# Kernel tuning notes

Measured on AMD Instinct MI355X. Metric: run time of the kernel, lower is better.

## Reference

```python
import jax, jax.numpy as jnp
import numpy as np
from jax import lax

BINS = 256
HSIG = 0.01
MS_WEIGHTS = np.array([0.0448, 0.2856, 0.3001, 0.2363, 0.1333], dtype=np.float32)


def _conv(x, w, b=None, pad='SAME', groups=1):
    out = lax.conv_general_dilated(x, w, (1, 1), pad,
                                   feature_group_count=groups,
                                   dimension_numbers=('NCHW', 'OIHW', 'NCHW'))
    if b is not None:
        out = out + b[None, :, None, None]
    return out


def _avg_pool(x, k):
    B, C, H, W = x.shape
    return x.reshape(B, C, H // k, k, W // k, k).mean(axis=(3, 5))


def _max_pool2(x):
    return lax.reduce_window(x, -jnp.inf, lax.max, (1, 1, 2, 2), (1, 1, 2, 2), 'VALID')


def _gauss_win():
    c = jnp.arange(11, dtype=jnp.float32) - 5.0
    g = jnp.exp(-(c * c) / (2.0 * 1.5 * 1.5))
    return g / g.sum()


def _gauss_filter(x, win):
    C = x.shape[1]
    wh = jnp.tile(win.reshape(1, 1, 11, 1), (C, 1, 1, 1))
    ww = jnp.tile(win.reshape(1, 1, 1, 11), (C, 1, 1, 1))
    x = _conv(x, wh, pad='VALID', groups=C)
    return _conv(x, ww, pad='VALID', groups=C)


def _ssim(X, Y, win):
    C1, C2 = 0.01 ** 2, 0.03 ** 2
    mu1 = _gauss_filter(X, win)
    mu2 = _gauss_filter(Y, win)
    s11 = _gauss_filter(X * X, win) - mu1 * mu1
    s22 = _gauss_filter(Y * Y, win) - mu2 * mu2
    s12 = _gauss_filter(X * Y, win) - mu1 * mu2
    cs = (2.0 * s12 + C2) / (s11 + s22 + C2)
    ssim = ((2.0 * mu1 * mu2 + C1) / (mu1 * mu1 + mu2 * mu2 + C1)) * cs
    return ssim.mean(axis=(2, 3)), cs.mean(axis=(2, 3))  # (B,C) each


def _ms_ssim(X, Y):
    win = _gauss_win()
    vals = []
    for i in range(5):
        s, c = _ssim(X, Y, win)
        vals.append(jax.nn.relu(s if i == 4 else c))
        if i < 4:
            X = _avg_pool(X, 2)
            Y = _avg_pool(Y, 2)
    v = jnp.stack(vals)  # (5,B,C)
    w = jnp.asarray(MS_WEIGHTS)[:, None, None]
    return jnp.prod(v ** w, axis=0).mean()


def _soft_hist(y, edges):
    # faithful to source: broadcast every pixel against 256 Gaussian bins,
    # sum over dim 0 (batch), then normalize to a distribution.
    h = jnp.exp(-0.5 * ((y[..., None] - edges) / HSIG) ** 2).sum(axis=0)  # (C,H,W,BINS)
    return h / h.sum()


def _vgg_feats(x, ws, bs):
    # VGG19 features[:16]: conv1_1..conv3_3, maxpool after conv idx 1 and 3.
    for i, (w, b) in enumerate(zip(ws, bs)):
        x = jax.nn.relu(_conv(x, w, b))
        if i in (1, 3):
            x = _max_pool2(x)
    return x


def combined_loss(y_true, y_pred, ws, bs):
    B, C, H, W = y_pred.shape
    diff = y_pred - y_true
    ad = jnp.abs(diff)
    # smooth L1 (beta=1)
    l1 = jnp.mean(jnp.where(ad < 1.0, 0.5 * diff * diff, ad - 0.5))
    # MS-SSIM loss
    msssim_l = 1.0 - _ms_ssim(y_true, y_pred)
    # VGG perceptual
    f1 = _vgg_feats(y_true, ws, bs)
    f2 = _vgg_feats(y_pred, ws, bs)
    perc = jnp.mean((f1 - f2) ** 2)
    # soft histogram
    edges = jnp.linspace(0.0, 1.0, BINS, dtype=jnp.float32)
    hist_l = jnp.mean(jnp.abs(_soft_hist(y_true, edges) - _soft_hist(y_pred, edges)))
    # PSNR loss: 40 - (-10*log10(mse))
    mse = jnp.mean(diff * diff)
    psnr_l = 40.0 + 10.0 * jnp.log10(mse)
    # color loss
    color_l = jnp.mean(jnp.abs(y_true.mean(axis=(1, 2, 3)) - y_pred.mean(axis=(1, 2, 3))))
    # exposure loss (16x16 avg pool of channel mean, target 0.6)
    exp_l = jnp.mean((_avg_pool(y_pred.mean(axis=1, keepdims=True), 16) - 0.6) ** 2)
    # illumination smoothness (counts faithful to source)
    hv = jnp.sum((y_pred[:, :, 1:, :] - y_pred[:, :, :-1, :]) ** 2)
    wv = jnp.sum((y_pred[:, :, :, 1:] - y_pred[:, :, :, :-1]) ** 2)
    ill = 2.0 * (hv / ((W - 1) * C) + wv / (W * (C - 1))) / B
    # spatial consistency: 4 neighbor-difference kernels on 4x4-pooled luminance
    K = jnp.array([[[0, 0, 0], [-1, 1, 0], [0, 0, 0]],
                   [[0, 0, 0], [0, 1, -1], [0, 0, 0]],
                   [[0, -1, 0], [0, 1, 0], [0, 0, 0]],
                   [[0, 0, 0], [0, 1, 0], [0, -1, 0]]], dtype=jnp.float32)[:, None]  # (4,1,3,3)
    op = _avg_pool(y_true.mean(axis=1, keepdims=True), 4)
    ep = _avg_pool(y_pred.mean(axis=1, keepdims=True), 4)
    spat = jnp.sum((_conv(op, K) - _conv(ep, K)) ** 2, axis=1, keepdims=True)  # (B,1,H/4,W/4)
    total = (1.0 * l1 + 0.06 * perc + 0.05 * hist_l + 0.0083 * psnr_l
             + 0.25 * color_l + 0.5 * msssim_l + 0.1 * exp_l + 0.1 * ill + 0.1 * spat)
    return jnp.mean(total)


def setup_inputs() -> dict:
    key = jax.random.key(0)
    ks = jax.random.split(key, 16)
    B, H, W = 2, 224, 224
    y_true = jax.random.uniform(ks[0], (B, 3, H, W), dtype=jnp.float32)
    y_pred = jax.random.uniform(ks[1], (B, 3, H, W), dtype=jnp.float32)
    chans = [(64, 3), (64, 64), (128, 64), (128, 128), (256, 128), (256, 256), (256, 256)]
    inp = {'y_true': y_true, 'y_pred': y_pred}
    for i, (co, ci) in enumerate(chans):
        std = float(np.sqrt(2.0 / (ci * 9)))
        inp[f'w{i}'] = jax.random.normal(ks[2 + i], (co, ci, 3, 3), dtype=jnp.float32) * std
        inp[f'b{i}'] = jnp.zeros((co,), dtype=jnp.float32)
    return inp


def reference(y_true, y_pred, w0, w1, w2, w3, w4, w5, w6, b0, b1, b2, b3, b4, b5, b6):
    ws = [w0, w1, w2, w3, w4, w5, w6]
    bs = [b0, b1, b2, b3, b4, b5, b6]
    return combined_loss(y_true, y_pred, ws, bs)
```

## Files before the change

### kernel.cpp

```cpp
#include <hip/hip_runtime.h>
#include <cmath>

typedef __attribute__((ext_vector_type(8))) short  short8;
typedef __attribute__((ext_vector_type(4))) float  floatx4;
typedef __attribute__((ext_vector_type(8))) unsigned short ushort8;
typedef __attribute__((ext_vector_type(8))) unsigned char uchar8v;

#define SLOT(i) ((i) * 16)
#define ACC_L1   0
#define ACC_MSE  1
#define ACC_ST0  2
#define ACC_ST1  3
#define ACC_SP0  4
#define ACC_SP1  5
#define ACC_HV   6
#define ACC_WV   7
#define ACC_EXP  8
#define ACC_SPAT 9
#define ACC_PERC 10
#define SSIM_SLOT(scale, cs, img) (256 + ((scale) * 12 + (cs) * 6 + (img)) * 16)
#define ZPAGE_FLOAT_OFF 3200

struct GW { float g[11]; };

__device__ __forceinline__ float waveSum(float v) {
#pragma unroll
  for (int o = 32; o > 0; o >>= 1) v += __shfl_down(v, o, 64);
  return v;
}

__device__ __forceinline__ float blockSum256(float v) {
  __shared__ float red[4];
  const int tid = threadIdx.x;
  v = waveSum(v);
  __syncthreads();
  if ((tid & 63) == 0) red[tid >> 6] = v;
  __syncthreads();
  return red[0] + red[1] + red[2] + red[3];
}

__device__ __forceinline__ unsigned int pk_fp8x4(float v0, float v1, float v2, float v3) {
  int p = __builtin_amdgcn_cvt_pk_fp8_f32(v0, v1, 0, false);
  p = __builtin_amdgcn_cvt_pk_fp8_f32(v2, v3, p, true);
  return (unsigned int)p;
}

__device__ __forceinline__ void gload16(const unsigned char* g, unsigned char* l) {
  __builtin_amdgcn_global_load_lds(
      (const __attribute__((address_space(1))) void*)g,
      (__attribute__((address_space(3))) void*)l, 16, 0, 0);
}

__device__ __forceinline__ void ssim_tile(
    int bid, int img, const float* __restrict__ yt, const float* __restrict__ yp,
    const float* __restrict__ pyrX, const float* __restrict__ pyrY,
    float* __restrict__ acc, const GW& gw,
    float (*sX)[27], float (*sY)[27], float (*sV)[16][27]) {
  int s = 0;
  if (bid >= 196) s = 1;
  if (bid >= 245) s = 2;
  if (bid >= 254) s = 3;
  if (bid >= 258) s = 4;
  const int cumA[5]   = {0, 196, 245, 254, 258};
  const int tilesA[5] = {14, 7, 3, 2, 1};
  const int dimsA[5]  = {224, 112, 56, 28, 14};
  const int offsA[5]  = {0, 0, 75264, 94080, 98784};
  const int t = bid - cumA[s];
  const int tiles = tilesA[s];
  const int n = dimsA[s];
  const int m = n - 10;
  const int tid = threadIdx.x;
  const int ty0 = (t / tiles) * 16;
  const int tx0 = (t - (t / tiles) * tiles) * 16;
  const float* Xb = ((s == 0) ? yt : pyrX + offsA[s]) + (size_t)img * n * n;
  const float* Yb = ((s == 0) ? yp : pyrY + offsA[s]) + (size_t)img * n * n;

  for (int e = tid; e < 26 * 26; e += 256) {
    const int r = e / 26, c = e - (e / 26) * 26;
    const int gy = ty0 + r, gx = tx0 + c;
    float xv = 0.f, yv = 0.f;
    if (gy < n && gx < n) {
      xv = Xb[(size_t)gy * n + gx];
      yv = Yb[(size_t)gy * n + gx];
    }
    sX[r][c] = xv; sY[r][c] = yv;
  }
  __syncthreads();

  for (int e = tid; e < 16 * 26; e += 256) {
    const int r = e / 26, c = e - (e / 26) * 26;
    float sx = 0.f, sy = 0.f, sxx = 0.f, syy = 0.f, sxy = 0.f;
#pragma unroll
    for (int tt = 0; tt < 11; ++tt) {
      const float xv = sX[r + tt][c];
      const float yv = sY[r + tt][c];
      const float g = gw.g[tt];
      sx += g * xv; sy += g * yv;
      sxx += g * xv * xv; syy += g * yv * yv; sxy += g * xv * yv;
    }
    sV[0][r][c] = sx; sV[1][r][c] = sy;
    sV[2][r][c] = sxx; sV[3][r][c] = syy; sV[4][r][c] = sxy;
  }
  __syncthreads();

  float sv = 0.f, cv = 0.f;
  {
    const int r = tid >> 4, c = tid & 15;
    if (ty0 + r < m && tx0 + c < m) {
      float mu1 = 0.f, mu2 = 0.f, e11 = 0.f, e22 = 0.f, e12 = 0.f;
#pragma unroll
      for (int tt = 0; tt < 11; ++tt) {
        const float g = gw.g[tt];
        mu1 += g * sV[0][r][c + tt];
        mu2 += g * sV[1][r][c + tt];
        e11 += g * sV[2][r][c + tt];
        e22 += g * sV[3][r][c + tt];
        e12 += g * sV[4][r][c + tt];
      }
      const float C1 = 1e-4f, C2 = 9e-4f;
      const float s11 = e11 - mu1 * mu1;
      const float s22 = e22 - mu2 * mu2;
      const float s12 = e12 - mu1 * mu2;
      cv = (2.f * s12 + C2) / (s11 + s22 + C2);
      sv = ((2.f * mu1 * mu2 + C1) / (mu1 * mu1 + mu2 * mu2 + C1)) * cv;
    }
  }
  float tsum = blockSum256(sv);
  if (tid == 0) atomicAdd(acc + SSIM_SLOT(s, 0, img), tsum);
  tsum = blockSum256(cv);
  if (tid == 0) atomicAdd(acc + SSIM_SLOT(s, 1, img), tsum);
}


struct PrepArgs {
  const float* w[6];
  int co[6], ci[6];
  int wcum[7];
  unsigned char* zp[6];
  int zH[6];
  int zcum[7];
};

struct MegaArgs {
  PrepArgs pa;
  unsigned char* wdst;
  const float* w0;
  const float* b0;
  unsigned char* c1;
  float* pyrX;
  float* pyrY;
  float* acc;
  int nPrep, nBasic, nPyr, nPS, nW4;
};

__global__ __launch_bounds__(256) void mega_k(MegaArgs A,
                                              const float* __restrict__ yt,
                                              const float* __restrict__ yp) {
  __shared__ float smem[684];
  const int tid = threadIdx.x;
  int bid = blockIdx.x;

  if (bid < A.nPrep) {
    const int idx = bid * 256 + tid;
    const PrepArgs& a = A.pa;
    if (idx < A.nW4) {
      const int e0 = idx * 4;
      int L = 0;
      while (e0 >= a.wcum[L + 1]) ++L;
      const int r = e0 - a.wcum[L];
      const int Cin = a.ci[L];
      const int cin = r % Cin;
      const int t = r / Cin;
      const int tap = t % 9;
      const int cout = t / 9;
      const float* wsrc = a.w[L] + ((size_t)cout * Cin + cin) * 9 + tap;
      *(unsigned int*)(A.wdst + e0) =
          pk_fp8x4(wsrc[0] * 8.f, wsrc[9] * 8.f, wsrc[18] * 8.f, wsrc[27] * 8.f);
      return;
    }
    const int zi = idx - A.nW4;
    if (zi >= a.zcum[6]) return;
    int b = 0;
    while (zi >= a.zcum[b + 1]) ++b;
    const int H = a.zH[b];
    const int rowE = (H + 2) * 32;
    const int perC = (2 * rowE + 2 * H * 32) >> 4;
    const int k = zi - a.zcum[b];
    const int pl = k / perC;
    const int k0 = (k - pl * perC) << 4;
    size_t o;
    if (k0 < rowE) o = k0;
    else if (k0 < 2 * rowE) o = (size_t)(H + 1) * rowE + (k0 - rowE);
    else {
      const int kk = k0 - 2 * rowE;
      const int y = kk / 64 + 1;
      const int r = kk & 63;
      o = (size_t)y * rowE + ((r < 32) ? (size_t)r : ((size_t)(H + 1) * 32 + (r - 32)));
    }
    *(uint4*)(a.zp[b] + (size_t)pl * (H + 2) * rowE + o) = (uint4){0, 0, 0, 0};
    return;
  }
  bid -= A.nPrep;

  if (bid < A.nBasic) {
    float* acc = A.acc;
    const int i4 = bid * 256 + tid;
    const int idx = i4 * 4;
    const float4 t4 = *(const float4*)(yt + idx);
    const float4 p4 = *(const float4*)(yp + idx);
    float l1 = 0.f, mse = 0.f, st0 = 0.f, st1 = 0.f, sp0 = 0.f, sp1 = 0.f, hv = 0.f, wv = 0.f;
#define BTERM(tt, pp) { const float d = (pp) - (tt); const float ad = fabsf(d); \
                        l1 += (ad < 1.f) ? 0.5f * d * d : ad - 0.5f; mse += d * d; }
    BTERM(t4.x, p4.x) BTERM(t4.y, p4.y) BTERM(t4.z, p4.z) BTERM(t4.w, p4.w)
#undef BTERM
    const float ts = t4.x + t4.y + t4.z + t4.w;
    const float ps = p4.x + p4.y + p4.z + p4.w;
    if (i4 < 37632) { st0 = ts; sp0 = ps; } else { st1 = ts; sp1 = ps; }
    const int h = (idx / 224) % 224;
    if (h < 223) {
      const float4 pn = *(const float4*)(yp + idx + 224);
      float d;
      d = pn.x - p4.x; hv += d * d;
      d = pn.y - p4.y; hv += d * d;
      d = pn.z - p4.z; hv += d * d;
      d = pn.w - p4.w; hv += d * d;
    }
    {
      const int w = idx % 224;
      float d;
      d = p4.y - p4.x; wv += d * d;
      d = p4.z - p4.y; wv += d * d;
      d = p4.w - p4.z; wv += d * d;
      if (w < 220) { d = yp[idx + 4] - p4.w; wv += d * d; }
    }
    float s;
    s = blockSum256(l1);  if (tid == 0) atomicAdd(acc + SLOT(ACC_L1), s);
    s = blockSum256(mse); if (tid == 0) atomicAdd(acc + SLOT(ACC_MSE), s);
    s = blockSum256(st0); if (tid == 0) atomicAdd(acc + SLOT(ACC_ST0), s);
    s = blockSum256(st1); if (tid == 0) atomicAdd(acc + SLOT(ACC_ST1), s);
    s = blockSum256(sp0); if (tid == 0) atomicAdd(acc + SLOT(ACC_SP0), s);
    s = blockSum256(sp1); if (tid == 0) atomicAdd(acc + SLOT(ACC_SP1), s);
    s = blockSum256(hv);  if (tid == 0) atomicAdd(acc + SLOT(ACC_HV), s);
    s = blockSum256(wv);  if (tid == 0) atomicAdd(acc + SLOT(ACC_WV), s);
    return;
  }
  bid -= A.nBasic;

  if (bid < A.nPyr) {
    float (*sA)[17] = (float(*)[17])smem;
    float (*s1)[9]  = (float(*)[9])(smem + 272);
    float (*s2)[5]  = (float(*)[5])(smem + 344);
    float (*s3)[3]  = (float(*)[3])(smem + 364);
    const int tile = bid % 196;
    const int img = (bid / 196) % 6;
    const int zt = bid / (196 * 6);
    const int ty = tile / 14, tx = tile - ty * 14;
    const float* src = (zt ? yp : yt) + (size_t)img * 224 * 224;
    float* dst = zt ? A.pyrY : A.pyrX;
    const int r = tid >> 4, c = tid & 15;
    sA[r][c] = src[(size_t)(ty * 16 + r) * 224 + tx * 16 + c];
    __syncthreads();
    if (tid < 64) {
      const int r1 = tid >> 3, c1 = tid & 7;
      const float m = 0.25f * (sA[2 * r1][2 * c1] + sA[2 * r1][2 * c1 + 1] +
                               sA[2 * r1 + 1][2 * c1] + sA[2 * r1 + 1][2 * c1 + 1]);
      dst[(size_t)img * 12544 + (ty * 8 + r1) * 112 + tx * 8 + c1] = m;
      s1[r1][c1] = m;
    }
    __syncthreads();
    if (tid < 16) {
      const int r2 = tid >> 2, c2 = tid & 3;
      const float m = 0.25f * (s1[2 * r2][2 * c2] + s1[2 * r2][2 * c2 + 1] +
                               s1[2 * r2 + 1][2 * c2] + s1[2 * r2 + 1][2 * c2 + 1]);
      dst[75264 + (size_t)img * 3136 + (ty * 4 + r2) * 56 + tx * 4 + c2] = m;
      s2[r2][c2] = m;
    }
    __syncthreads();
    if (tid < 4) {
      const int r3 = tid >> 1, c3 = tid & 1;
      const float m = 0.25f * (s2[2 * r3][2 * c3] + s2[2 * r3][2 * c3 + 1] +
                               s2[2 * r3 + 1][2 * c3] + s2[2 * r3 + 1][2 * c3 + 1]);
      dst[94080 + (size_t)img * 784 + (ty * 2 + r3) * 28 + tx * 2 + c3] = m;
      s3[r3][c3] = m;
    }
    __syncthreads();
    if (tid == 0) {
      const float m = 0.25f * (s3[0][0] + s3[0][1] + s3[1][0] + s3[1][1]);
      dst[98784 + (size_t)img * 196 + ty * 14 + tx] = m;
    }
    return;
  }
  bid -= A.nPyr;

  if (bid < A.nPS) {
    float* acc = A.acc;
    float (*sOp)[19] = (float(*)[19])smem;
    float (*sEp)[19] = (float(*)[19])(smem + 342);
    const int b = bid >> 4;
    const int tq = bid & 15;
    const int ty0 = (tq >> 2) * 16, tx0 = (tq & 3) * 16;
    for (int e = tid; e < 18 * 18; e += 256) {
      const int r = e / 18, c = e - (e / 18) * 18;
      const int gy = ty0 - 1 + r, gx = tx0 - 1 + c;
      float vo = 0.f, ve = 0.f;
      if (gy >= 0 && gy < 56 && gx >= 0 && gx < 56) {
        float so = 0.f, se = 0.f;
        for (int ch = 0; ch < 3; ++ch)
#pragma unroll
          for (int dy = 0; dy < 4; ++dy) {
            const size_t off = (((size_t)b * 3 + ch) * 224 + (gy * 4 + dy)) * 224 + gx * 4;
            const float4 a = *(const float4*)(yt + off);
            const float4 ee = *(const float4*)(yp + off);
            so += a.x + a.y + a.z + a.w;
            se += ee.x + ee.y + ee.z + ee.w;
          }
        vo = so * (1.f / 48.f);
        ve = se * (1.f / 48.f);
      }
      sOp[r][c] = vo; sEp[r][c] = ve;
    }
    __syncthreads();
    float v = 0.f;
    {
      const int r = tid >> 4, c = tid & 15;
      const int gy = ty0 + r, gx = tx0 + c;
      if (gy < 56 && gx < 56) {
        const float oc = sOp[r + 1][c + 1], ec = sEp[r + 1][c + 1];
        const float ol = sOp[r + 1][c],     el = sEp[r + 1][c];
        const float orr = sOp[r + 1][c + 2], er = sEp[r + 1][c + 2];
        const float ou = sOp[r][c + 1],     eu = sEp[r][c + 1];
        const float od = sOp[r + 2][c + 1], ed = sEp[r + 2][c + 1];
        float d;
        d = (oc - ol) - (ec - el);   v += d * d;
        d = (oc - orr) - (ec - er);  v += d * d;
        d = (oc - ou) - (ec - eu);   v += d * d;
        d = (oc - od) - (ec - ed);   v += d * d;
      }
    }
    const float t = blockSum256(v);
    if (tid == 0) atomicAdd(acc + SLOT(ACC_SPAT), t);
    if (tid < 16) {
      const int ey = tid >> 2, ex = tid & 3;
      if (ty0 + 4 * ey < 56 && tx0 + 4 * ex < 56) {
        float ssum = 0.f;
#pragma unroll
        for (int dy = 0; dy < 4; ++dy)
#pragma unroll
          for (int dx = 0; dx < 4; ++dx)
            ssum += sEp[4 * ey + dy + 1][4 * ex + dx + 1];
        const float m = ssum * (1.f / 16.f) - 0.6f;
        atomicAdd(acc + SLOT(ACC_EXP), m * m);
      }
    }
    return;
  }
  bid -= A.nPS;

  {
    float (*sIn)[10][12] = (float(*)[10][12])smem;
    const int zf = bid / 784;
    const int rem = bid - zf * 784;
    const int by = rem / 28, bx = rem - by * 28;
    const int tx = tid & 7, ty = (tid >> 3) & 7, tz = tid >> 6;
    const int img = zf >> 1;
    const int zb = zf & 1;
    const float* in = ((img >> 1) ? yp : yt) + (size_t)(img & 1) * 3 * 224 * 224;
    const int x0 = bx << 3, y0 = by << 3;
    const int x = x0 + tx, y = y0 + ty;
    int wrow = (zb * 32 + tz * 8) * 27;
    wrow = __builtin_amdgcn_readfirstlane(wrow);

    for (int el = tid; el < 300; el += 256) {
      const int ci = el / 100;
      const int r2 = el - ci * 100;
      const int r = r2 / 10, cl = r2 - r * 10;
      const int gy = y0 - 1 + r, gx = x0 - 1 + cl;
      float v = 0.f;
      if (gy >= 0 && gy < 224 && gx >= 0 && gx < 224)
        v = in[((size_t)ci * 224 + gy) * 224 + gx];
      sIn[ci][r][cl] = v;
    }
    __syncthreads();

    float a[8];
#pragma unroll
    for (int j = 0; j < 8; ++j) a[j] = 0.f;
#pragma unroll
    for (int ci = 0; ci < 3; ++ci) {
      float xv[9];
#pragma unroll
      for (int ky = 0; ky < 3; ++ky)
#pragma unroll
        for (int kx = 0; kx < 3; ++kx)
          xv[ky * 3 + kx] = sIn[ci][ty + ky][tx + kx];
      const float* wp = A.w0 + wrow + ci * 9;
#pragma unroll
      for (int j = 0; j < 8; ++j)
#pragma unroll
        for (int k = 0; k < 9; ++k)
          a[j] = fmaf(xv[k], wp[27 * j + k], a[j]);
    }
    const int coB = zb * 32 + tz * 8;
    float r[8];
#pragma unroll
    for (int j = 0; j < 8; ++j) r[j] = fmaxf(a[j] + A.b0[coB + j], 0.f);
    const size_t o = (((size_t)(zb * 4 + img) * 226 + (y + 1)) * 226 + (x + 1)) * 32 + tz * 8;
    uint2 rv;
    rv.x = pk_fp8x4(r[0], r[1], r[2], r[3]);
    rv.y = pk_fp8x4(r[4], r[5], r[6], r[7]);
    *(uint2*)(A.c1 + o) = rv;
  }
}

template<int CIN, bool DB, bool POOL>
__global__ __launch_bounds__(256, (DB ? 2 : 4)) void conv_mfma(
    const unsigned char* __restrict__ in, const unsigned char* __restrict__ wtp,
    const float* __restrict__ bias, unsigned char* __restrict__ out,
    const float* __restrict__ zpage, int W, int rowsPI) {
  constexpr int NSLAB = CIN / 32;
  constexpr int NBUF = DB ? 2 : 1;
  constexpr int ASTB = 304;
  constexpr int BSTB = 48;
  constexpr int NBRUN = 6 * 66;
  constexpr int NPX = 66;
  constexpr int ASLOT = 32 * 19;
  constexpr int BSLOT = NBRUN * 3;
  constexpr int NAI = 3;
  constexpr int NBI = 5;
  __shared__ __align__(16) unsigned char As[NBUF][32 * ASTB];
  __shared__ __align__(16) unsigned char Bs[NBUF][NBRUN * BSTB];

  const int tid = threadIdx.x;
  const int lane = tid & 63;
  const int wave = tid >> 6;
  const int quad = lane >> 4;
  const int lr = lane & 15;
  const int img = blockIdx.y / rowsPI;
  const int y0 = (blockIdx.y - img * rowsPI) * 4;
  const int x0 = blockIdx.x * 64;
  const int cob = blockIdx.z * 32;
  const int Wp = W + 2;
  const int H = rowsPI * 4;
  const size_t IPL = (size_t)(H + 2) * Wp * 32;
  const unsigned char* inI = in + (size_t)img * IPL;
  const int Wo = W >> 1, Ho = H >> 1;
  const size_t OPL = POOL ? (size_t)(Ho + 2) * (Wo + 2) * 32 : IPL;
  unsigned char* outI = out + ((size_t)blockIdx.z * 4 + img) * OPL;

  floatx4 acc[2][4];
#pragma unroll
  for (int m = 0; m < 2; ++m)
#pragma unroll
    for (int n = 0; n < 4; ++n) acc[m][n] = (floatx4){0.f, 0.f, 0.f, 0.f};

  const int abase = lr * ASTB + quad * 8;

  const unsigned char* aptr[NAI];
  bool aok[NAI];
#pragma unroll
  for (int i = 0; i < NAI; ++i) {
    const int sl = tid + i * 256;
    aok[i] = sl < ASLOT;
    const int cout = aok[i] ? (sl / 19) : 0;
    const int r = sl - cout * 19;
    const int rr = (r >= 18) ? 17 : r;
    const int tap = rr >> 1, part = rr & 1;
    aptr[i] = wtp + ((size_t)(cob + cout) * 9 + tap) * CIN + part * 16;
  }
  const unsigned char* bptr[NBI];
  unsigned int bstep[NBI];
  bool bok[NBI];
#pragma unroll
  for (int i = 0; i < NBI; ++i) {
    const int sl = tid + i * 256;
    bok[i] = sl < BSLOT;
    const int run = sl / 3;
    const int r = sl - run * 3;
    const int part = (r >= 2) ? 1 : r;
    const int row = run / NPX;
    const int px = run - row * NPX;
    const int gx = x0 + px;
    if (bok[i] && gx < Wp) {
      bptr[i] = inI + ((size_t)(y0 + row) * Wp + gx) * 32 + part * 16;
      bstep[i] = (unsigned int)(4 * IPL);
    } else {
      bptr[i] = (const unsigned char*)zpage;
      bstep[i] = 0;
    }
  }

  auto stage = [&](int buf) {
#pragma unroll
    for (int i = 0; i < NAI; ++i)
      if (aok[i]) {
        gload16(aptr[i], As[buf] + (tid + i * 256) * 16);
        aptr[i] += 32;
      }
#pragma unroll
    for (int i = 0; i < NBI; ++i)
      if (bok[i]) {
        gload16(bptr[i], Bs[buf] + (tid + i * 256) * 16);
        bptr[i] += bstep[i];
      }
  };

  auto mfma_slab = [&](int buf) {
#pragma unroll
    for (int dy = 0; dy < 3; ++dy)
#pragma unroll
      for (int dx = 0; dx < 3; ++dx) {
        const int tap = dy * 3 + dx;
        const long af0 = *(const long*)(As[buf] + abase + tap * 32);
        const long af1 = *(const long*)(As[buf] + abase + 16 * ASTB + tap * 32);
        long bfr[4];
#pragma unroll
        for (int n = 0; n < 4; ++n)
          bfr[n] = *(const long*)(Bs[buf] + ((wave + dy) * NPX + n * 16 + lr + dx) * BSTB + quad * 8);
#pragma unroll
        for (int n = 0; n < 4; ++n) {
          acc[0][n] = __builtin_amdgcn_mfma_f32_16x16x32_fp8_fp8(af0, bfr[n], acc[0][n], 0, 0, 0);
          acc[1][n] = __builtin_amdgcn_mfma_f32_16x16x32_fp8_fp8(af1, bfr[n], acc[1][n], 0, 0, 0);
        }
      }
  };

  if constexpr (!DB) {
    for (int s = 0; s < NSLAB; ++s) {
      __syncthreads();
      stage(0);
      __syncthreads();
      mfma_slab(0);
    }
  } else {
    stage(0);
    __syncthreads();
    for (int s = 0; s < NSLAB; ++s) {
      const int cur = s & 1;
      if (s + 1 < NSLAB) stage(cur ^ 1);
      mfma_slab(cur);
      __syncthreads();
    }
  }

  if constexpr (!POOL) {
#pragma unroll
    for (int m = 0; m < 2; ++m) {
      const int cb = cob + m * 16 + quad * 4;
#pragma unroll
      for (int n = 0; n < 4; ++n) {
        const int px = x0 + n * 16 + lr;
        if (px < W) {
          const float v0 = fmaxf(acc[m][n].x * 0.125f + bias[cb + 0], 0.f);
          const float v1 = fmaxf(acc[m][n].y * 0.125f + bias[cb + 1], 0.f);
          const float v2 = fmaxf(acc[m][n].z * 0.125f + bias[cb + 2], 0.f);
          const float v3 = fmaxf(acc[m][n].w * 0.125f + bias[cb + 3], 0.f);
          *(unsigned int*)(outI + ((size_t)(y0 + wave + 1) * Wp + px + 1) * 32 +
                           m * 16 + quad * 4) = pk_fp8x4(v0, v1, v2, v3);
        }
      }
    }
  } else {
    __syncthreads();
    unsigned char* sT = Bs[0];
#pragma unroll
    for (int m = 0; m < 2; ++m) {
      const int cb = cob + m * 16 + quad * 4;
#pragma unroll
      for (int n = 0; n < 4; ++n) {
        const int px = n * 16 + lr;
        const float v0 = fmaxf(acc[m][n].x * 0.125f + bias[cb + 0], 0.f);
        const float v1 = fmaxf(acc[m][n].y * 0.125f + bias[cb + 1], 0.f);
        const float v2 = fmaxf(acc[m][n].z * 0.125f + bias[cb + 2], 0.f);
        const float v3 = fmaxf(acc[m][n].w * 0.125f + bias[cb + 3], 0.f);
        *(unsigned int*)(sT + ((wave * 64 + px) * 32 + m * 16 + quad * 4)) =
            pk_fp8x4(v0, v1, v2, v3);
      }
    }
    __syncthreads();
    const int ch8 = (tid & 3) * 8;
    const int co = (tid >> 2) & 31;
    const int ro = tid >> 7;
    const int pxo = (x0 >> 1) + co;
    if (pxo < Wo) {
      const uchar8v a = *(const uchar8v*)(sT + ((2 * ro) * 64 + 2 * co) * 32 + ch8);
      const uchar8v b = *(const uchar8v*)(sT + ((2 * ro) * 64 + 2 * co + 1) * 32 + ch8);
      const uchar8v c = *(const uchar8v*)(sT + ((2 * ro + 1) * 64 + 2 * co) * 32 + ch8);
      const uchar8v d = *(const uchar8v*)(sT + ((2 * ro + 1) * 64 + 2 * co + 1) * 32 + ch8);
      const uchar8v r = __builtin_elementwise_max(__builtin_elementwise_max(a, b),
                                                  __builtin_elementwise_max(c, d));
      *(uchar8v*)(outI + ((size_t)((y0 >> 1) + ro + 1) * (Wo + 2) + (pxo + 1)) * 32 + ch8) = r;
    }
  }
}

__global__ __launch_bounds__(256, 4) void conv2_ssim_k(
    const unsigned char* __restrict__ in, const unsigned char* __restrict__ wtp,
    const float* __restrict__ bias, unsigned char* __restrict__ out,
    const float* __restrict__ zpage,
    const float* __restrict__ yt, const float* __restrict__ yp,
    const float* __restrict__ pyrX, const float* __restrict__ pyrY,
    float* __restrict__ acc_g, GW gw) {
  constexpr int CIN = 64;
  constexpr int NSLAB = CIN / 32;
  constexpr int ASTB = 304;
  constexpr int BSTB = 48;
  constexpr int NBRUN = 6 * 66;
  constexpr int NPX = 66;
  constexpr int ASLOT = 32 * 19;
  constexpr int BSLOT = NBRUN * 3;
  constexpr int NAI = 3;
  constexpr int NBI = 5;
  const int W = 224, rowsPI = 56;
  __shared__ __align__(16) unsigned char As[32 * ASTB];
  __shared__ __align__(16) unsigned char Bs[NBRUN * BSTB];

  const int tid = threadIdx.x;

  if (blockIdx.z >= 2) {
    const int sid = (blockIdx.z - 2) * 896 + blockIdx.y * 4 + blockIdx.x;
    if (sid >= 1554) return;
    const int img = sid / 259;
    const int bid = sid - img * 259;
    float (*sX)[27] = (float(*)[27])As;
    float (*sY)[27] = (float(*)[27])(As + 2816);
    float (*sV)[16][27] = (float(*)[16][27])Bs;
    ssim_tile(bid, img, yt, yp, pyrX, pyrY, acc_g, gw, sX, sY, sV);
    return;
  }

  const int lane = tid & 63;
  const int wave = tid >> 6;
  const int quad = lane >> 4;
  const int lr = lane & 15;
  const int img = blockIdx.y / rowsPI;
  const int y0 = (blockIdx.y - img * rowsPI) * 4;
  const int x0 = blockIdx.x * 64;
  const int cob = blockIdx.z * 32;
  const int Wp = W + 2;
  const int H = rowsPI * 4;
  const size_t IPL = (size_t)(H + 2) * Wp * 32;
  const int Wo = W >> 1, Ho = H >> 1;
  const size_t OPL = (size_t)(Ho + 2) * (Wo + 2) * 32;
  const unsigned char* inI = in + (size_t)img * IPL;
  unsigned char* outI = out + ((size_t)blockIdx.z * 4 + img) * OPL;

  floatx4 acc[2][4];
#pragma unroll
  for (int m = 0; m < 2; ++m)
#pragma unroll
    for (int n = 0; n < 4; ++n) acc[m][n] = (floatx4){0.f, 0.f, 0.f, 0.f};

  const int abase = lr * ASTB + quad * 8;

  const unsigned char* aptr[NAI];
  bool aok[NAI];
#pragma unroll
  for (int i = 0; i < NAI; ++i) {
    const int sl = tid + i * 256;
    aok[i] = sl < ASLOT;
    const int cout = aok[i] ? (sl / 19) : 0;
    const int r = sl - cout * 19;
    const int rr = (r >= 18) ? 17 : r;
    const int tap = rr >> 1, part = rr & 1;
    aptr[i] = wtp + ((size_t)(cob + cout) * 9 + tap) * CIN + part * 16;
  }
  const unsigned char* bptr[NBI];
  unsigned int bstep[NBI];
  bool bok[NBI];
#pragma unroll
  for (int i = 0; i < NBI; ++i) {
    const int sl = tid + i * 256;
    bok[i] = sl < BSLOT;
    const int run = sl / 3;
    const int r = sl - run * 3;
    const int part = (r >= 2) ? 1 : r;
    const int row = run / NPX;
    const int px = run - row * NPX;
    const int gx = x0 + px;
    if (bok[i] && gx < Wp) {
      bptr[i] = inI + ((size_t)(y0 + row) * Wp + gx) * 32 + part * 16;
      bstep[i] = (unsigned int)(4 * IPL);
    } else {
      bptr[i] = (const unsigned char*)zpage;
      bstep[i] = 0;
    }
  }

  for (int s = 0; s < NSLAB; ++s) {
    __syncthreads();
#pragma unroll
    for (int i = 0; i < NAI; ++i)
      if (aok[i]) {
        gload16(aptr[i], As + (tid + i * 256) * 16);
        aptr[i] += 32;
      }
#pragma unroll
    for (int i = 0; i < NBI; ++i)
      if (bok[i]) {
        gload16(bptr[i], Bs + (tid + i * 256) * 16);
        bptr[i] += bstep[i];
      }
    __syncthreads();

#pragma unroll
    for (int dy = 0; dy < 3; ++dy)
#pragma unroll
      for (int dx = 0; dx < 3; ++dx) {
        const int tap = dy * 3 + dx;
        const long af0 = *(const long*)(As + abase + tap * 32);
        const long af1 = *(const long*)(As + abase + 16 * ASTB + tap * 32);
        long bfr[4];
#pragma unroll
        for (int n = 0; n < 4; ++n)
          bfr[n] = *(const long*)(Bs + ((wave + dy) * NPX + n * 16 + lr + dx) * BSTB + quad * 8);
#pragma unroll
        for (int n = 0; n < 4; ++n) {
          acc[0][n] = __builtin_amdgcn_mfma_f32_16x16x32_fp8_fp8(af0, bfr[n], acc[0][n], 0, 0, 0);
          acc[1][n] = __builtin_amdgcn_mfma_f32_16x16x32_fp8_fp8(af1, bfr[n], acc[1][n], 0, 0, 0);
        }
      }
  }

  __syncthreads();
  unsigned char* sT = Bs;
#pragma unroll
  for (int m = 0; m < 2; ++m) {
    const int cb = cob + m * 16 + quad * 4;
#pragma unroll
    for (int n = 0; n < 4; ++n) {
      const int px = n * 16 + lr;
      const float v0 = fmaxf(acc[m][n].x * 0.125f + bias[cb + 0], 0.f);
      const float v1 = fmaxf(acc[m][n].y * 0.125f + bias[cb + 1], 0.f);
      const float v2 = fmaxf(acc[m][n].z * 0.125f + bias[cb + 2], 0.f);
      const float v3 = fmaxf(acc[m][n].w * 0.125f + bias[cb + 3], 0.f);
      *(unsigned int*)(sT + ((wave * 64 + px) * 32 + m * 16 + quad * 4)) =
          pk_fp8x4(v0, v1, v2, v3);
    }
  }
  __syncthreads();
  const int ch8 = (tid & 3) * 8;
  const int co = (tid >> 2) & 31;
  const int ro = tid >> 7;
  const int pxo = (x0 >> 1) + co;
  if (pxo < Wo) {
    const uchar8v a = *(const uchar8v*)(sT + ((2 * ro) * 64 + 2 * co) * 32 + ch8);
    const uchar8v b = *(const uchar8v*)(sT + ((2 * ro) * 64 + 2 * co + 1) * 32 + ch8);
    const uchar8v c = *(const uchar8v*)(sT + ((2 * ro + 1) * 64 + 2 * co) * 32 + ch8);
    const uchar8v d = *(const uchar8v*)(sT + ((2 * ro + 1) * 64 + 2 * co + 1) * 32 + ch8);
    const uchar8v r = __builtin_elementwise_max(__builtin_elementwise_max(a, b),
                                                __builtin_elementwise_max(c, d));
    *(uchar8v*)(outI + ((size_t)((y0 >> 1) + ro + 1) * (Wo + 2) + (pxo + 1)) * 32 + ch8) = r;
  }
}

#define FP8D(av, bv, J) { const float dd = __builtin_amdgcn_cvt_f32_fp8((av), (J)) - \
                                           __builtin_amdgcn_cvt_f32_fp8((bv), (J)); \
                          v = fmaf(dd, dd, v); }
__global__ __launch_bounds__(256) void perc_k(const unsigned char* __restrict__ f,
                                              float* __restrict__ acc) {
  const int PER = 56 * 56 * 256 / 8;
  const size_t PL = (size_t)58 * 58 * 32;
  float v = 0.f;
  for (int ch = blockIdx.x * 256 + threadIdx.x; ch < 2 * PER; ch += 256 * 256) {
    const int q = ch / PER;
    const int r = ch - q * PER;
    const int e = r * 8;
    const int c = e & 255;
    const int p = e >> 8;
    const int x = p % 56, y = p / 56;
    const int zb = c >> 5;
    const int cw = c & 31;
    const size_t o = (size_t)(zb * 4 + q) * PL + ((size_t)(y + 1) * 58 + (x + 1)) * 32 + cw;
    const uint2 a = *(const uint2*)(f + o);
    const uint2 b = *(const uint2*)(f + o + 2 * PL);
    FP8D(a.x, b.x, 0) FP8D(a.x, b.x, 1) FP8D(a.x, b.x, 2) FP8D(a.x, b.x, 3)
    FP8D(a.y, b.y, 0) FP8D(a.y, b.y, 1) FP8D(a.y, b.y, 2) FP8D(a.y, b.y, 3)
  }
  const float t = blockSum256(v);
  if (threadIdx.x == 0) atomicAdd(acc + SLOT(ACC_PERC), t);
}

__global__ void final_k(const float* __restrict__ acc, float* __restrict__ out) {
  if (threadIdx.x != 0 || blockIdx.x != 0) return;
  const float NPIX = 2.f * 3.f * 224.f * 224.f;
  const float l1 = acc[SLOT(ACC_L1)] / NPIX;
  const float mse = acc[SLOT(ACC_MSE)] / NPIX;
  const float psnr = 40.f + 10.f * log10f(mse);
  const float cm = 1.f / (3.f * 224.f * 224.f);
  const float color = 0.5f * (fabsf(acc[SLOT(ACC_ST0)] - acc[SLOT(ACC_SP0)]) +
                              fabsf(acc[SLOT(ACC_ST1)] - acc[SLOT(ACC_SP1)])) * cm;
  const float ill = acc[SLOT(ACC_HV)] / 669.f + acc[SLOT(ACC_WV)] / 448.f;
  const float expl = acc[SLOT(ACC_EXP)] / 392.f;
  const float spat = acc[SLOT(ACC_SPAT)] / 6272.f;
  const float perc = acc[SLOT(ACC_PERC)] / 1605632.f;
  const float wms[5] = {0.0448f, 0.2856f, 0.3001f, 0.2363f, 0.1333f};
  const int ns[5] = {214, 102, 46, 18, 4};
  float msum = 0.f;
  for (int img = 0; img < 6; ++img) {
    float prod = 1.f;
    for (int s = 0; s < 5; ++s) {
      const float denom = (float)(ns[s] * ns[s]);
      float v = (s == 4) ? acc[SSIM_SLOT(s, 0, img)] / denom
                         : acc[SSIM_SLOT(s, 1, img)] / denom;
      v = fmaxf(v, 0.f);
      prod *= powf(v, wms[s]);
    }
    msum += prod;
  }
  const float msssim = msum / 6.f;
  out[0] = l1 + 0.06f * perc + 0.0083f * psnr + 0.25f * color +
           0.5f * (1.f - msssim) + 0.1f * expl + 0.1f * ill + 0.1f * spat;
}

extern "C" void kernel_launch(void* const* d_in, const int* in_sizes, int n_in,
                              void* d_out, int out_size, void* d_ws, size_t ws_size,
                              hipStream_t stream) {
  const float* yt = (const float*)d_in[0];
  const float* yp = (const float*)d_in[1];
  const float* W7[7]; const float* B7[7];
  for (int i = 0; i < 7; ++i) {
    W7[i] = (const float*)d_in[2 + 2 * i];
    B7[i] = (const float*)d_in[3 + 2 * i];
  }

  char* ws = (char*)d_ws;
  float* acc = (float*)ws;
  const float* zpage = acc + ZPAGE_FLOAT_OFF;
  size_t off = 16384;
  auto align256 = [&]() { off = (off + 255) & ~(size_t)255; };
  align256(); unsigned char* C1  = (unsigned char*)(ws + off); off += (size_t)4 * 226 * 226 * 64;
  align256(); unsigned char* T0  = (unsigned char*)(ws + off); off += (size_t)4 * 226 * 226 * 64;
  align256(); unsigned char* Pl1 = (unsigned char*)(ws + off); off += (size_t)4 * 114 * 114 * 64;
  align256(); unsigned char* C3  = (unsigned char*)(ws + off); off += (size_t)4 * 114 * 114 * 128;
  align256(); unsigned char* Pl2 = (unsigned char*)(ws + off); off += (size_t)4 * 58 * 58 * 128;
  align256(); unsigned char* C5  = (unsigned char*)(ws + off); off += (size_t)4 * 58 * 58 * 256;
  align256(); unsigned char* C6  = (unsigned char*)(ws + off); off += (size_t)4 * 58 * 58 * 256;
  align256(); unsigned char* F   = (unsigned char*)(ws + off); off += (size_t)4 * 58 * 58 * 256;
  align256(); unsigned char* WT  = (unsigned char*)(ws + off); off += (size_t)1732608;
  align256(); float* pyrX = (float*)(ws + off); off += (size_t)100000 * 4;
  align256(); float* pyrY = (float*)(ws + off); off += (size_t)100000 * 4;
  if (ws_size < off) return;
  (void)T0;

  GW gw;
  {
    double vv[11]; double s = 0.0;
    for (int i = 0; i < 11; ++i) { const double c = i - 5.0; vv[i] = exp(-(c * c) / 4.5); s += vv[i]; }
    for (int i = 0; i < 11; ++i) gw.g[i] = (float)(vv[i] / s);
  }

  hipMemsetAsync(acc, 0, 16384, stream);

  const int co[7] = {64, 64, 128, 128, 256, 256, 256};
  const int ci[7] = {3, 64, 64, 128, 128, 256, 256};
  MegaArgs ma;
  size_t wtOff[7];
  {
    int e = 0;
    for (int i = 1; i < 7; ++i) {
      ma.pa.w[i - 1] = W7[i]; ma.pa.co[i - 1] = co[i]; ma.pa.ci[i - 1] = ci[i];
      ma.pa.wcum[i - 1] = e; wtOff[i] = (size_t)e; e += co[i] * 9 * ci[i];
    }
    ma.pa.wcum[6] = e;
    ma.nW4 = e / 4;
    unsigned char* bufs[6] = {C1, Pl1, C3, Pl2, C5, C6};
    const int hh[6] = {224, 112, 112, 56, 56, 56};
    const int cc[6] = {64, 64, 128, 128, 256, 256};
    int z = 0;
    for (int i = 0; i < 6; ++i) {
      ma.pa.zp[i] = bufs[i]; ma.pa.zH[i] = hh[i];
      ma.pa.zcum[i] = z;
      const int perC = (2 * (hh[i] + 2) * 32 + 2 * hh[i] * 32) >> 4;
      z += (4 * cc[i] / 32) * perC;
    }
    ma.pa.zcum[6] = z;
    ma.nPrep = (ma.nW4 + z + 255) / 256;
  }
  ma.wdst = WT;
  ma.w0 = W7[0]; ma.b0 = B7[0];
  ma.c1 = C1;
  ma.pyrX = pyrX; ma.pyrY = pyrY;
  ma.acc = acc;
  ma.nBasic = 294;
  ma.nPyr = 196 * 6 * 2;
  ma.nPS = 32;
  const int nConv1 = 28 * 28 * 8;
  const int megaBlocks = ma.nPrep + ma.nBasic + ma.nPyr + ma.nPS + nConv1;

  mega_k<<<megaBlocks, 256, 0, stream>>>(ma, yt, yp);

  conv2_ssim_k<<<dim3(4, 224, 4), 256, 0, stream>>>(
      C1, WT + wtOff[1], B7[1], Pl1, zpage, yt, yp, pyrX, pyrY, acc, gw);
  conv_mfma<64, false, false> <<<dim3(2, 4 * 28, 4), 256, 0, stream>>>(Pl1, WT + wtOff[2], B7[2], C3, zpage, 112, 28);
  conv_mfma<128, false, true> <<<dim3(2, 4 * 28, 4), 256, 0, stream>>>(C3,  WT + wtOff[3], B7[3], Pl2, zpage, 112, 28);
  conv_mfma<128, true, false> <<<dim3(1, 4 * 14, 8), 256, 0, stream>>>(Pl2, WT + wtOff[4], B7[4], C5, zpage, 56, 14);
  conv_mfma<256, true, false> <<<dim3(1, 4 * 14, 8), 256, 0, stream>>>(C5,  WT + wtOff[5], B7[5], C6, zpage, 56, 14);
  conv_mfma<256, true, false> <<<dim3(1, 4 * 14, 8), 256, 0, stream>>>(C6,  WT + wtOff[6], B7[6], F,  zpage, 56, 14);
  perc_k<<<256, 256, 0, stream>>>(F, acc);

  final_k<<<1, 64, 0, stream>>>(acc, (float*)d_out);
}
```

Measured before the change: 252.9 us.

## Move SSIM tiles into deep conv layers, double-buffer slabs, fuse final reduction

The SSIM tile work is moved off the large conv2 kernel and split across the three 56x56 deep conv launches (518 tiles each). Those launches are under-occupied, so the SSIM blocks fill idle CUs there. conv2 becomes a plain conv_mfma launch with fused pooling. The deep conv kernel gets double-buffered LDS staging so slab loads overlap the MFMA work, at lower occupancy (launch_bounds 2). The final scalar reduction is folded into the perceptual kernel using a last-block atomic counter, which removes one launch. The counter relies on the memset of the accumulator region.

Result: slower. 258.1 us (+2.1%).

```diff
diff --git a/kernel.cpp b/kernel.cpp
--- a/kernel.cpp
+++ b/kernel.cpp
@@ -18,6 +18,7 @@
 #define ACC_EXP  8
 #define ACC_SPAT 9
 #define ACC_PERC 10
+#define CNT_OFF  240
 #define SSIM_SLOT(scale, cs, img) (256 + ((scale) * 12 + (cs) * 6 + (img)) * 16)
 #define ZPAGE_FLOAT_OFF 3200
 
@@ -593,14 +594,14 @@
   }
 }
 
-__global__ __launch_bounds__(256, 4) void conv2_ssim_k(
+template<int CIN>
+__global__ __launch_bounds__(256, 2) void conv_deep_ssim_k(
     const unsigned char* __restrict__ in, const unsigned char* __restrict__ wtp,
     const float* __restrict__ bias, unsigned char* __restrict__ out,
     const float* __restrict__ zpage,
     const float* __restrict__ yt, const float* __restrict__ yp,
     const float* __restrict__ pyrX, const float* __restrict__ pyrY,
-    float* __restrict__ acc_g, GW gw) {
-  constexpr int CIN = 64;
+    float* __restrict__ acc_g, GW gw, int tileBase, int nTiles) {
   constexpr int NSLAB = CIN / 32;
   constexpr int ASTB = 304;
   constexpr int BSTB = 48;
@@ -610,20 +611,21 @@
   constexpr int BSLOT = NBRUN * 3;
   constexpr int NAI = 3;
   constexpr int NBI = 5;
-  const int W = 224, rowsPI = 56;
-  __shared__ __align__(16) unsigned char As[32 * ASTB];
-  __shared__ __align__(16) unsigned char Bs[NBRUN * BSTB];
+  const int W = 56, rowsPI = 14;
+  __shared__ __align__(16) unsigned char As[2][32 * ASTB];
+  __shared__ __align__(16) unsigned char Bs[2][NBRUN * BSTB];
 
   const int tid = threadIdx.x;
 
-  if (blockIdx.z >= 2) {
-    const int sid = (blockIdx.z - 2) * 896 + blockIdx.y * 4 + blockIdx.x;
-    if (sid >= 1554) return;
-    const int img = sid / 259;
-    const int bid = sid - img * 259;
-    float (*sX)[27] = (float(*)[27])As;
-    float (*sY)[27] = (float(*)[27])(As + 2816);
-    float (*sV)[16][27] = (float(*)[16][27])Bs;
+  if (blockIdx.z >= 8) {
+    const int sl = (blockIdx.z - 8) * 56 + blockIdx.y;
+    if (sl >= nTiles) return;
+    const int tile = tileBase + sl;
+    const int img = tile / 259;
+    const int bid = tile - img * 259;
+    float (*sX)[27] = (float(*)[27])&As[0][0];
+    float (*sY)[27] = (float(*)[27])(&As[0][0] + 2816);
+    float (*sV)[16][27] = (float(*)[16][27])&Bs[0][0];
     ssim_tile(bid, img, yt, yp, pyrX, pyrY, acc_g, gw, sX, sY, sV);
     return;
   }
@@ -639,10 +641,8 @@
   const int Wp = W + 2;
   const int H = rowsPI * 4;
   const size_t IPL = (size_t)(H + 2) * Wp * 32;
-  const int Wo = W >> 1, Ho = H >> 1;
-  const size_t OPL = (size_t)(Ho + 2) * (Wo + 2) * 32;
   const unsigned char* inI = in + (size_t)img * IPL;
-  unsigned char* outI = out + ((size_t)blockIdx.z * 4 + img) * OPL;
+  unsigned char* outI = out + ((size_t)blockIdx.z * 4 + img) * IPL;
 
   floatx4 acc[2][4];
 #pragma unroll
@@ -686,78 +686,74 @@
     }
   }
 
-  for (int s = 0; s < NSLAB; ++s) {
-    __syncthreads();
+  auto stage = [&](int buf) {
 #pragma unroll
     for (int i = 0; i < NAI; ++i)
       if (aok[i]) {
-        gload16(aptr[i], As + (tid + i * 256) * 16);
+        gload16(aptr[i], As[buf] + (tid + i * 256) * 16);
         aptr[i] += 32;
       }
 #pragma unroll
     for (int i = 0; i < NBI; ++i)
       if (bok[i]) {
-        gload16(bptr[i], Bs + (tid + i * 256) * 16);
+        gload16(bptr[i], Bs[buf] + (tid + i * 256) * 16);
         bptr[i] += bstep[i];
       }
-    __syncthreads();
-
+  };
+
+  auto mfma_slab = [&](int buf) {
 #pragma unroll
     for (int dy = 0; dy < 3; ++dy)
 #pragma unroll
       for (int dx = 0; dx < 3; ++dx) {
         const int tap = dy * 3 + dx;
-        const long af0 = *(const long*)(As + abase + tap * 32);
-        const long af1 = *(const long*)(As + abase + 16 * ASTB + tap * 32);
+        const long af0 = *(const long*)(As[buf] + abase + tap * 32);
+        const long af1 = *(const long*)(As[buf] + abase + 16 * ASTB + tap * 32);
         long bfr[4];
 #pragma unroll
         for (int n = 0; n < 4; ++n)
-          bfr[n] = *(const long*)(Bs + ((wave + dy) * NPX + n * 16 + lr + dx) * BSTB + quad * 8);
+          bfr[n] = *(const long*)(Bs[buf] + ((wave + dy) * NPX + n * 16 + lr + dx) * BSTB + quad * 8);
 #pragma unroll
         for (int n = 0; n < 4; ++n) {
           acc[0][n] = __builtin_amdgcn_mfma_f32_16x16x32_fp8_fp8(af0, bfr[n], acc[0][n], 0, 0, 0);
           acc[1][n] = __builtin_amdgcn_mfma_f32_16x16x32_fp8_fp8(af1, bfr[n], acc[1][n], 0, 0, 0);
         }
       }
-  }
-
+  };
+
+  stage(0);
   __syncthreads();
-  unsigned char* sT = Bs;
+  for (int s = 0; s < NSLAB; ++s) {
+    const int cur = s & 1;
+    if (s + 1 < NSLAB) stage(cur ^ 1);
+    mfma_slab(cur);
+    __syncthreads();
+  }
+
 #pragma unroll
   for (int m = 0; m < 2; ++m) {
     const int cb = cob + m * 16 + quad * 4;
 #pragma unroll
     for (int n = 0; n < 4; ++n) {
-      const int px = n * 16 + lr;
-      const float v0 = fmaxf(acc[m][n].x * 0.125f + bias[cb + 0], 0.f);
-      const float v1 = fmaxf(acc[m][n].y * 0.125f + bias[cb + 1], 0.f);
-      const float v2 = fmaxf(acc[m][n].z * 0.125f + bias[cb + 2], 0.f);
-      const float v3 = fmaxf(acc[m][n].w * 0.125f + bias[cb + 3], 0.f);
-      *(unsigned int*)(sT + ((wave * 64 + px) * 32 + m * 16 + quad * 4)) =
-          pk_fp8x4(v0, v1, v2, v3);
-    }
-  }
-  __syncthreads();
-  const int ch8 = (tid & 3) * 8;
-  const int co = (tid >> 2) & 31;
-  const int ro = tid >> 7;
-  const int pxo = (x0 >> 1) + co;
-  if (pxo < Wo) {
-    const uchar8v a = *(const uchar8v*)(sT + ((2 * ro) * 64 + 2 * co) * 32 + ch8);
-    const uchar8v b = *(const uchar8v*)(sT + ((2 * ro) * 64 + 2 * co + 1) * 32 + ch8);
-    const uchar8v c = *(const uchar8v*)(sT + ((2 * ro + 1) * 64 + 2 * co) * 32 + ch8);
-    const uchar8v d = *(const uchar8v*)(sT + ((2 * ro + 1) * 64 + 2 * co + 1) * 32 + ch8);
-    const uchar8v r = __builtin_elementwise_max(__builtin_elementwise_max(a, b),
-                                                __builtin_elementwise_max(c, d));
-    *(uchar8v*)(outI + ((size_t)((y0 >> 1) + ro + 1) * (Wo + 2) + (pxo + 1)) * 32 + ch8) = r;
+      const int px = x0 + n * 16 + lr;
+      if (px < W) {
+        const float v0 = fmaxf(acc[m][n].x * 0.125f + bias[cb + 0], 0.f);
+        const float v1 = fmaxf(acc[m][n].y * 0.125f + bias[cb + 1], 0.f);
+        const float v2 = fmaxf(acc[m][n].z * 0.125f + bias[cb + 2], 0.f);
+        const float v3 = fmaxf(acc[m][n].w * 0.125f + bias[cb + 3], 0.f);
+        *(unsigned int*)(outI + ((size_t)(y0 + wave + 1) * Wp + px + 1) * 32 +
+                         m * 16 + quad * 4) = pk_fp8x4(v0, v1, v2, v3);
+      }
+    }
   }
 }
 
 #define FP8D(av, bv, J) { const float dd = __builtin_amdgcn_cvt_f32_fp8((av), (J)) - \
                                            __builtin_amdgcn_cvt_f32_fp8((bv), (J)); \
                           v = fmaf(dd, dd, v); }
-__global__ __launch_bounds__(256) void perc_k(const unsigned char* __restrict__ f,
-                                              float* __restrict__ acc) {
+__global__ __launch_bounds__(256) void perc_final_k(const unsigned char* __restrict__ f,
+                                                    float* __restrict__ acc,
+                                                    float* __restrict__ out) {
   const int PER = 56 * 56 * 256 / 8;
   const size_t PL = (size_t)58 * 58 * 32;
   float v = 0.f;
@@ -777,11 +773,13 @@
     FP8D(a.y, b.y, 0) FP8D(a.y, b.y, 1) FP8D(a.y, b.y, 2) FP8D(a.y, b.y, 3)
   }
   const float t = blockSum256(v);
-  if (threadIdx.x == 0) atomicAdd(acc + SLOT(ACC_PERC), t);
-}
-
-__global__ void final_k(const float* __restrict__ acc, float* __restrict__ out) {
-  if (threadIdx.x != 0 || blockIdx.x != 0) return;
+  if (threadIdx.x != 0) return;
+  atomicAdd(acc + SLOT(ACC_PERC), t);
+  __threadfence();
+  unsigned int* cnt = (unsigned int*)(acc + CNT_OFF);
+  const unsigned done = atomicAdd(cnt, 1u);
+  if (done != 255) return;
+
   const float NPIX = 2.f * 3.f * 224.f * 224.f;
   const float l1 = acc[SLOT(ACC_L1)] / NPIX;
   const float mse = acc[SLOT(ACC_MSE)] / NPIX;
@@ -800,10 +798,10 @@
     float prod = 1.f;
     for (int s = 0; s < 5; ++s) {
       const float denom = (float)(ns[s] * ns[s]);
-      float v = (s == 4) ? acc[SSIM_SLOT(s, 0, img)] / denom
-                         : acc[SSIM_SLOT(s, 1, img)] / denom;
-      v = fmaxf(v, 0.f);
-      prod *= powf(v, wms[s]);
+      float vv = (s == 4) ? acc[SSIM_SLOT(s, 0, img)] / denom
+                          : acc[SSIM_SLOT(s, 1, img)] / denom;
+      vv = fmaxf(vv, 0.f);
+      prod *= powf(vv, wms[s]);
     }
     msum += prod;
   }
@@ -829,7 +827,6 @@
   size_t off = 16384;
   auto align256 = [&]() { off = (off + 255) & ~(size_t)255; };
   align256(); unsigned char* C1  = (unsigned char*)(ws + off); off += (size_t)4 * 226 * 226 * 64;
-  align256(); unsigned char* T0  = (unsigned char*)(ws + off); off += (size_t)4 * 226 * 226 * 64;
   align256(); unsigned char* Pl1 = (unsigned char*)(ws + off); off += (size_t)4 * 114 * 114 * 64;
   align256(); unsigned char* C3  = (unsigned char*)(ws + off); off += (size_t)4 * 114 * 114 * 128;
   align256(); unsigned char* Pl2 = (unsigned char*)(ws + off); off += (size_t)4 * 58 * 58 * 128;
@@ -840,7 +837,6 @@
   align256(); float* pyrX = (float*)(ws + off); off += (size_t)100000 * 4;
   align256(); float* pyrY = (float*)(ws + off); off += (size_t)100000 * 4;
   if (ws_size < off) return;
-  (void)T0;
 
   GW gw;
   {
@@ -889,14 +885,14 @@
 
   mega_k<<<megaBlocks, 256, 0, stream>>>(ma, yt, yp);
 
-  conv2_ssim_k<<<dim3(4, 224, 4), 256, 0, stream>>>(
-      C1, WT + wtOff[1], B7[1], Pl1, zpage, yt, yp, pyrX, pyrY, acc, gw);
+  conv_mfma<64, false, true>  <<<dim3(4, 224, 2), 256, 0, stream>>>(C1,  WT + wtOff[1], B7[1], Pl1, zpage, 224, 56);
   conv_mfma<64, false, false> <<<dim3(2, 4 * 28, 4), 256, 0, stream>>>(Pl1, WT + wtOff[2], B7[2], C3, zpage, 112, 28);
   conv_mfma<128, false, true> <<<dim3(2, 4 * 28, 4), 256, 0, stream>>>(C3,  WT + wtOff[3], B7[3], Pl2, zpage, 112, 28);
-  conv_mfma<128, true, false> <<<dim3(1, 4 * 14, 8), 256, 0, stream>>>(Pl2, WT + wtOff[4], B7[4], C5, zpage, 56, 14);
-  conv_mfma<256, true, false> <<<dim3(1, 4 * 14, 8), 256, 0, stream>>>(C5,  WT + wtOff[5], B7[5], C6, zpage, 56, 14);
-  conv_mfma<256, true, false> <<<dim3(1, 4 * 14, 8), 256, 0, stream>>>(C6,  WT + wtOff[6], B7[6], F,  zpage, 56, 14);
-  perc_k<<<256, 256, 0, stream>>>(F, acc);
-
-  final_k<<<1, 64, 0, stream>>>(acc, (float*)d_out);
-}
+  conv_deep_ssim_k<128><<<dim3(1, 56, 18), 256, 0, stream>>>(
+      Pl2, WT + wtOff[4], B7[4], C5, zpage, yt, yp, pyrX, pyrY, acc, gw, 0, 518);
+  conv_deep_ssim_k<256><<<dim3(1, 56, 18), 256, 0, stream>>>(
+      C5, WT + wtOff[5], B7[5], C6, zpage, yt, yp, pyrX, pyrY, acc, gw, 518, 518);
+  conv_deep_ssim_k<256><<<dim3(1, 56, 18), 256, 0, stream>>>(
+      C6, WT + wtOff[6], B7[6], F, zpage, yt, yp, pyrX, pyrY, acc, gw, 1036, 518);
+  perc_final_k<<<256, 256, 0, stream>>>(F, acc, (float*)d_out);
+}
```
